# Performance work log

Hardware: AMD Instinct MI355X
Metric: run time of the kernel (lower is better)

Reference implementation:

```python
import jax, jax.numpy as jnp
import numpy as np

N = 65536      # total nodes
E = 262144     # directed edges
G = 2048       # graphs in batch
H = 512        # hidden_channels
HEADS = 2
DESC = 256


def setup_inputs() -> dict:
    key = jax.random.key(0)
    ks = jax.random.split(key, 18)
    w = lambda k, shape: (jax.random.normal(k, shape, jnp.float32) * 0.05)
    x = jax.random.normal(ks[0], (N, 9), jnp.float32)
    edge_index = jax.random.randint(ks[1], (2, E), 0, N)
    batch_index = (jnp.arange(N) * G) // N  # sorted graph ids, every graph non-empty
    descriptors = jax.random.normal(ks[2], (G, DESC), jnp.float32)
    return dict(
        x=x, edge_index=edge_index, batch_index=batch_index, descriptors=descriptors,
        gin_w=w(ks[3], (H, 9)), gin_b=w(ks[4], (H,)),
        gat_w=w(ks[5], (HEADS * H, H)), gat_asrc=w(ks[6], (HEADS, H)),
        gat_adst=w(ks[7], (HEADS, H)), gat_bias=w(ks[8], (H,)),
        sage_wl=w(ks[9], (H, H)), sage_bl=w(ks[10], (H,)), sage_wr=w(ks[11], (H, H)),
        fc_w=w(ks[12], (512, 2 * H + DESC)), fc_b=w(ks[13], (512,)),
        a1_w=w(ks[14], (256, 512)), a1_b=w(ks[15], (256,)),
        a2_w=w(ks[16], (1, 256)), a2_b=w(ks[17], (1,)),
    )


def reference(x, edge_index, batch_index, descriptors,
              gin_w, gin_b, gat_w, gat_asrc, gat_adst, gat_bias,
              sage_wl, sage_bl, sage_wr, fc_w, fc_b, a1_w, a1_b, a2_w, a2_b):
    # Dropout layers are identity in eval mode.
    gelu = lambda t: jax.nn.gelu(t, approximate=False)
    src, dst = edge_index[0], edge_index[1]

    # --- GINConv: nn((1+eps)*x + sum_{j->i} x_j), eps=0 ---
    agg = jax.ops.segment_sum(x[src], dst, num_segments=N)
    h = gelu((x + agg) @ gin_w.T + gin_b)

    # --- GATConv (heads=2, concat=False, add_self_loops=True) ---
    z = (h @ gat_w.T).reshape(N, HEADS, H)               # [N, heads, H]
    sl = jnp.arange(N)
    s2 = jnp.concatenate([src, sl])                      # edges + self loops
    d2 = jnp.concatenate([dst, sl])
    a_s = jnp.sum(z * gat_asrc[None], axis=-1)           # [N, heads]
    a_d = jnp.sum(z * gat_adst[None], axis=-1)
    logit = jax.nn.leaky_relu(a_s[s2] + a_d[d2], 0.2)    # [E', heads]
    m = jax.ops.segment_max(logit, d2, num_segments=N)
    e = jnp.exp(logit - m[d2])
    denom = jax.ops.segment_sum(e, d2, num_segments=N)
    alpha = e / denom[d2]                                # edge softmax per dst
    out = jax.ops.segment_sum(alpha[:, :, None] * z[s2], d2, num_segments=N)
    h = gelu(out.mean(axis=1) + gat_bias)

    # --- SAGEConv: lin_l(mean_j h_j) + lin_r(h_i) ---
    cnt = jax.ops.segment_sum(jnp.ones((E,), h.dtype), dst, num_segments=N)
    mean_agg = jax.ops.segment_sum(h[src], dst, num_segments=N) / jnp.maximum(cnt, 1.0)[:, None]
    h = gelu(mean_agg @ sage_wl.T + sage_bl + h @ sage_wr.T)

    # --- global max/mean pool + heads ---
    pmax = jax.ops.segment_max(h, batch_index, num_segments=G)
    nodes_per_g = jax.ops.segment_sum(jnp.ones((N,), h.dtype), batch_index, num_segments=G)
    pmean = jax.ops.segment_sum(h, batch_index, num_segments=G) / nodes_per_g[:, None]
    combined = jnp.concatenate([pmax, pmean, descriptors], axis=1)  # [G, 2H+DESC]
    sf = gelu(combined @ fc_w.T + fc_b)
    z1 = gelu(sf @ a1_w.T + a1_b)
    return z1 @ a2_w.T + a2_b                             # [G, 1]
```

## Files before the change

kernel.cpp:

```cpp
#include <hip/hip_runtime.h>
#include <math.h>

#define N_NODES 65536
#define N_EDGES 262144
#define N_GRAPHS 2048
#define HDIM 512
#define DESCD 256

typedef unsigned short u16;
typedef __attribute__((ext_vector_type(8))) short bf16x8;
typedef __attribute__((ext_vector_type(8))) u16 u16x8;
typedef __attribute__((ext_vector_type(4))) float f32x4;

__device__ __forceinline__ float gelu_f(float x) {
    return 0.5f * x * (1.0f + erff(x * 0.70710678118654752f));
}
__device__ __forceinline__ float lrelu_f(float x) {
    return x > 0.0f ? x : 0.2f * x;
}
__device__ __forceinline__ float wave_reduce_sum(float v) {
#pragma unroll
    for (int off = 32; off > 0; off >>= 1) v += __shfl_down(v, off, 64);
    return v;
}

__device__ __forceinline__ float bf2f(u16 u) { return __uint_as_float(((unsigned)u) << 16); }
__device__ __forceinline__ u16 f2bf(float f) {
    unsigned u = __float_as_uint(f);
    unsigned r = (u >> 16) & 1u;
    return (u16)((u + 0x7fffu + r) >> 16);
}
__device__ __forceinline__ void ld8b(const u16* p, float o[8]) {
    ushort4 v0 = *(const ushort4*)p;
    ushort4 v1 = *(const ushort4*)(p + 4);
    o[0] = bf2f(v0.x); o[1] = bf2f(v0.y); o[2] = bf2f(v0.z); o[3] = bf2f(v0.w);
    o[4] = bf2f(v1.x); o[5] = bf2f(v1.y); o[6] = bf2f(v1.z); o[7] = bf2f(v1.w);
}
__device__ __forceinline__ void st8b(u16* p, const float o[8]) {
    ushort4 a, b;
    a.x = f2bf(o[0]); a.y = f2bf(o[1]); a.z = f2bf(o[2]); a.w = f2bf(o[3]);
    b.x = f2bf(o[4]); b.y = f2bf(o[5]); b.z = f2bf(o[6]); b.w = f2bf(o[7]);
    *(ushort4*)p = a; *(ushort4*)(p + 4) = b;
}

__global__ void k_zero(int* __restrict__ p, int n) {
    int i = blockIdx.x * blockDim.x + threadIdx.x;
    if (i < n) p[i] = 0;
}

__global__ void k_cvt(const float* __restrict__ src, u16* __restrict__ dst, int n) {
    int i = blockIdx.x * blockDim.x + threadIdx.x;
    if (i < n) dst[i] = f2bf(src[i]);
}

__global__ void k_count(const int* __restrict__ dst, int* __restrict__ deg) {
    int e = blockIdx.x * blockDim.x + threadIdx.x;
    if (e < N_EDGES) atomicAdd(&deg[dst[e]], 1);
}

__global__ __launch_bounds__(1024) void k_scan(const int* __restrict__ deg,
                                               int* __restrict__ indptr,
                                               int* __restrict__ cursor) {
    __shared__ int part[1024];
    int t = threadIdx.x;
    int base = t * 64;
    int s = 0;
    for (int i = 0; i < 64; i++) s += deg[base + i];
    part[t] = s;
    __syncthreads();
    for (int off = 1; off < 1024; off <<= 1) {
        int v = (t >= off) ? part[t - off] : 0;
        __syncthreads();
        part[t] += v;
        __syncthreads();
    }
    int run = (t == 0) ? 0 : part[t - 1];
    for (int i = 0; i < 64; i++) {
        int d = deg[base + i];
        indptr[base + i] = run;
        cursor[base + i] = run;
        run += d;
    }
    if (t == 1023) indptr[N_NODES] = run;
}

__global__ void k_fill(const int* __restrict__ src, const int* __restrict__ dst,
                       int* __restrict__ cursor, int* __restrict__ col) {
    int e = blockIdx.x * blockDim.x + threadIdx.x;
    if (e < N_EDGES) {
        int d = dst[e];
        int pos = atomicAdd(&cursor[d], 1);
        col[pos] = src[e];
    }
}

__global__ __launch_bounds__(256) void k_gin(const float* __restrict__ x,
                                             const int* __restrict__ indptr,
                                             const int* __restrict__ col,
                                             const float* __restrict__ gw,
                                             const float* __restrict__ gb,
                                             u16* __restrict__ h1) {
    __shared__ float w[HDIM * 9];
    __shared__ float b[HDIM];
    for (int idx = threadIdx.x; idx < HDIM * 9; idx += 256) w[idx] = gw[idx];
    for (int idx = threadIdx.x; idx < HDIM; idx += 256) b[idx] = gb[idx];
    __syncthreads();
    int wave = threadIdx.x >> 6, lane = threadIdx.x & 63;
    int i = blockIdx.x * 4 + wave;
    if (i >= N_NODES) return;
    float s[9];
#pragma unroll
    for (int k = 0; k < 9; k++) s[k] = x[i * 9 + k];
    int beg = indptr[i], end = indptr[i + 1];
    for (int e = beg; e < end; e++) {
        int j = col[e];
#pragma unroll
        for (int k = 0; k < 9; k++) s[k] += x[j * 9 + k];
    }
#pragma unroll
    for (int q = 0; q < 8; q++) {
        int c = q * 64 + lane;
        float acc = b[c];
#pragma unroll
        for (int k = 0; k < 9; k++) acc += s[k] * w[c * 9 + k];
        h1[(size_t)i * HDIM + c] = f2bf(gelu_f(acc));
    }
}

__global__ __launch_bounds__(256) void k_vproj(const float* __restrict__ gat_w,
                                               const float* __restrict__ asrc,
                                               const float* __restrict__ adst,
                                               float* __restrict__ vs,
                                               float* __restrict__ vd) {
    int h = blockIdx.x;
    int t = threadIdx.x;
    const float* W = gat_w + (size_t)h * HDIM * HDIM;
    float s0 = 0.f, s1 = 0.f, d0 = 0.f, d1 = 0.f;
    for (int c = 0; c < HDIM; c++) {
        float as = asrc[h * HDIM + c], ad = adst[h * HDIM + c];
        float w0 = W[(size_t)c * HDIM + t];
        float w1 = W[(size_t)c * HDIM + t + 256];
        s0 += as * w0; s1 += as * w1;
        d0 += ad * w0; d1 += ad * w1;
    }
    vs[h * HDIM + t] = s0; vs[h * HDIM + t + 256] = s1;
    vd[h * HDIM + t] = d0; vd[h * HDIM + t + 256] = d1;
}

__global__ __launch_bounds__(256) void k_coef(const u16* __restrict__ h1,
                                              const float* __restrict__ vs,
                                              const float* __restrict__ vd,
                                              float* __restrict__ a_s,
                                              float* __restrict__ a_d) {
    int wave = threadIdx.x >> 6, lane = threadIdx.x & 63;
    int i = blockIdx.x * 4 + wave;
    if (i >= N_NODES) return;
    float hv[8];
    ld8b(h1 + (size_t)i * HDIM + lane * 8, hv);
    float s0 = 0, d0 = 0, s1 = 0, d1 = 0;
#pragma unroll
    for (int r = 0; r < 8; r++) {
        int c = lane * 8 + r;
        s0 += hv[r] * vs[c];
        d0 += hv[r] * vd[c];
        s1 += hv[r] * vs[HDIM + c];
        d1 += hv[r] * vd[HDIM + c];
    }
    s0 = wave_reduce_sum(s0);
    d0 = wave_reduce_sum(d0);
    s1 = wave_reduce_sum(s1);
    d1 = wave_reduce_sum(d1);
    if (lane == 0) {
        a_s[i * 2] = s0; a_s[i * 2 + 1] = s1;
        a_d[i * 2] = d0; a_d[i * 2 + 1] = d1;
    }
}

__global__ __launch_bounds__(256) void k_gatagg(const u16* __restrict__ h1,
                                                const float* __restrict__ a_s,
                                                const float* __restrict__ a_d,
                                                const int* __restrict__ indptr,
                                                const int* __restrict__ col,
                                                u16* __restrict__ agg0,
                                                u16* __restrict__ agg1) {
    int wave = threadIdx.x >> 6, lane = threadIdx.x & 63;
    int i = blockIdx.x * 4 + wave;
    if (i >= N_NODES) return;
    int beg = indptr[i], end = indptr[i + 1];
    float ad0 = a_d[i * 2], ad1 = a_d[i * 2 + 1];
    float sl0 = expf(lrelu_f(a_s[i * 2] + ad0));
    float sl1 = expf(lrelu_f(a_s[i * 2 + 1] + ad1));
    float den0 = sl0, den1 = sl1;
    for (int e = beg; e < end; e++) {
        int j = col[e];
        den0 += expf(lrelu_f(a_s[j * 2] + ad0));
        den1 += expf(lrelu_f(a_s[j * 2 + 1] + ad1));
    }
    float inv0 = 0.5f / den0, inv1 = 0.5f / den1;
    float acc0[8], acc1[8], hv[8];
    ld8b(h1 + (size_t)i * HDIM + lane * 8, hv);
    {
        float w0 = sl0 * inv0, w1 = sl1 * inv1;
#pragma unroll
        for (int r = 0; r < 8; r++) { acc0[r] = w0 * hv[r]; acc1[r] = w1 * hv[r]; }
    }
    for (int e = beg; e < end; e++) {
        int j = col[e];
        float w0 = expf(lrelu_f(a_s[j * 2] + ad0)) * inv0;
        float w1 = expf(lrelu_f(a_s[j * 2 + 1] + ad1)) * inv1;
        ld8b(h1 + (size_t)j * HDIM + lane * 8, hv);
#pragma unroll
        for (int r = 0; r < 8; r++) { acc0[r] += w0 * hv[r]; acc1[r] += w1 * hv[r]; }
    }
    st8b(agg0 + (size_t)i * HDIM + lane * 8, acc0);
    st8b(agg1 + (size_t)i * HDIM + lane * 8, acc1);
}

template <bool DUAL, bool POOL, bool AF32>
__global__ __launch_bounds__(256) void k_mgemm(const void* __restrict__ A0v,
                                               const u16* __restrict__ W0,
                                               const void* __restrict__ A1v,
                                               const u16* __restrict__ W1,
                                               int K, const float* __restrict__ bias,
                                               u16* __restrict__ C, int ldc,
                                               float* __restrict__ comb) {
    __shared__ u16 sA[128 * 64];
    __shared__ u16 sB[128 * 64];
    int t = threadIdx.x;
    int wave = t >> 6, lane = t & 63;
    int wr = wave >> 1, wc = wave & 1;
    int l15 = lane & 15, l4 = lane >> 4;
    int bx, by;
    {
        int nwgx = gridDim.x;
        int nwg = nwgx * gridDim.y;
        int bid = blockIdx.y * nwgx + blockIdx.x;
        int q = nwg >> 3;
        int l = (bid & 7) * q + (bid >> 3);
        bx = l % nwgx;
        by = l / nwgx;
    }
    int row0 = by * 128;
    int c0 = bx * 128;

    f32x4 acc[4][4];
#pragma unroll
    for (int i = 0; i < 4; i++)
#pragma unroll
        for (int j = 0; j < 4; j++) acc[i][j] = (f32x4){0.f, 0.f, 0.f, 0.f};

    int half = K / 64;
    int nks = DUAL ? 2 * half : half;
    for (int ks = 0; ks < nks; ks++) {
        bool second = DUAL && (ks >= half);
        const u16* ApU = (const u16*)(second ? A1v : A0v);
        const float* ApF = (const float*)(second ? A1v : A0v);
        const u16* Wp = second ? W1 : W0;
        int k0 = (second ? (ks - half) : ks) * 64;
        u16x8 ga[4], gb[4];
#pragma unroll
        for (int q = 0; q < 4; q++) {
            int cid = q * 256 + t;
            int row = cid >> 3, cb = cid & 7;
            if constexpr (AF32) {
                const float* p = ApF + (size_t)(row0 + row) * K + k0 + cb * 8;
                float4 f0 = *(const float4*)p;
                float4 f1 = *(const float4*)(p + 4);
                u16x8 v;
                v[0] = f2bf(f0.x); v[1] = f2bf(f0.y); v[2] = f2bf(f0.z); v[3] = f2bf(f0.w);
                v[4] = f2bf(f1.x); v[5] = f2bf(f1.y); v[6] = f2bf(f1.z); v[7] = f2bf(f1.w);
                ga[q] = v;
            } else {
                ga[q] = *(const u16x8*)(ApU + (size_t)(row0 + row) * K + k0 + cb * 8);
            }
            gb[q] = *(const u16x8*)(Wp + (size_t)(c0 + row) * K + k0 + cb * 8);
        }
        __syncthreads();
#pragma unroll
        for (int q = 0; q < 4; q++) {
            int cid = q * 256 + t;
            int row = cid >> 3, cb = cid & 7;
            int sw = (cb ^ (row & 7)) * 8;
            *(u16x8*)(sA + row * 64 + sw) = ga[q];
            *(u16x8*)(sB + row * 64 + sw) = gb[q];
        }
        __syncthreads();
#pragma unroll
        for (int h = 0; h < 2; h++) {
            bf16x8 af[4], bfv[4];
            int cb = h * 4 + l4;
#pragma unroll
            for (int i = 0; i < 4; i++) {
                int ra = wr * 64 + i * 16 + l15;
                af[i] = *(const bf16x8*)(sA + ra * 64 + ((cb ^ (ra & 7)) * 8));
                int rb = wc * 64 + i * 16 + l15;
                bfv[i] = *(const bf16x8*)(sB + rb * 64 + ((cb ^ (rb & 7)) * 8));
            }
#pragma unroll
            for (int i = 0; i < 4; i++)
#pragma unroll
                for (int j = 0; j < 4; j++)
                    acc[i][j] = __builtin_amdgcn_mfma_f32_16x16x32_bf16(af[i], bfv[j], acc[i][j], 0, 0, 0);
        }
    }

    if constexpr (!POOL) {
#pragma unroll
        for (int i = 0; i < 4; i++) {
            int rbase = row0 + wr * 64 + i * 16 + l4 * 4;
#pragma unroll
            for (int j = 0; j < 4; j++) {
                int colc = c0 + wc * 64 + j * 16 + l15;
                float bv = bias[colc];
#pragma unroll
                for (int r = 0; r < 4; r++)
                    C[(size_t)(rbase + r) * ldc + colc] = f2bf(gelu_f(acc[i][j][r] + bv));
            }
        }
    } else {
#pragma unroll
        for (int gl = 0; gl < 2; gl++) {
            int g = (row0 >> 5) + wr * 2 + gl;
#pragma unroll
            for (int j = 0; j < 4; j++) {
                int colc = c0 + wc * 64 + j * 16 + l15;
                float bv = bias[colc];
                float mx = -1e30f, sm = 0.0f;
#pragma unroll
                for (int i = 0; i < 2; i++) {
#pragma unroll
                    for (int r = 0; r < 4; r++) {
                        float v = gelu_f(acc[gl * 2 + i][j][r] + bv);
                        mx = fmaxf(mx, v);
                        sm += v;
                    }
                }
                mx = fmaxf(mx, __shfl_xor(mx, 16, 64)); sm += __shfl_xor(sm, 16, 64);
                mx = fmaxf(mx, __shfl_xor(mx, 32, 64)); sm += __shfl_xor(sm, 32, 64);
                if (l4 == 0) {
                    comb[(size_t)g * 1280 + colc] = mx;
                    comb[(size_t)g * 1280 + 512 + colc] = sm * (1.0f / 32.0f);
                }
            }
        }
    }
}

__global__ __launch_bounds__(256) void k_sagemean(const u16* __restrict__ h2,
                                                  const int* __restrict__ indptr,
                                                  const int* __restrict__ col,
                                                  u16* __restrict__ mean) {
    int wave = threadIdx.x >> 6, lane = threadIdx.x & 63;
    int i = blockIdx.x * 4 + wave;
    if (i >= N_NODES) return;
    int beg = indptr[i], end = indptr[i + 1];
    float acc[8], hv[8];
#pragma unroll
    for (int r = 0; r < 8; r++) acc[r] = 0.0f;
    for (int e = beg; e < end; e++) {
        int j = col[e];
        ld8b(h2 + (size_t)j * HDIM + lane * 8, hv);
#pragma unroll
        for (int r = 0; r < 8; r++) acc[r] += hv[r];
    }
    float invc = 1.0f / fmaxf((float)(end - beg), 1.0f);
#pragma unroll
    for (int r = 0; r < 8; r++) acc[r] *= invc;
    st8b(mean + (size_t)i * HDIM + lane * 8, acc);
}

__global__ void k_desc(const float* __restrict__ desc, float* __restrict__ comb) {
    int idx = blockIdx.x * blockDim.x + threadIdx.x;
    int g = idx >> 8, c = idx & 255;
    comb[(size_t)g * 1280 + 1024 + c] = desc[(size_t)g * DESCD + c];
}

__global__ __launch_bounds__(256) void k_final(const u16* __restrict__ z1,
                                               const float* __restrict__ a2w,
                                               const float* __restrict__ a2b,
                                               float* __restrict__ out) {
    int wave = threadIdx.x >> 6, lane = threadIdx.x & 63;
    int g = blockIdx.x * 4 + wave;
    if (g >= N_GRAPHS) return;
    float s = 0.0f;
#pragma unroll
    for (int q = 0; q < 4; q++) {
        int c = q * 64 + lane;
        s += bf2f(z1[g * 256 + c]) * a2w[c];
    }
    s = wave_reduce_sum(s);
    if (lane == 0) out[g] = s + a2b[0];
}

extern "C" void kernel_launch(void* const* d_in, const int* in_sizes, int n_in,
                              void* d_out, int out_size, void* d_ws, size_t ws_size,
                              hipStream_t stream) {
    (void)in_sizes; (void)n_in;
    const float* x = (const float*)d_in[0];
    const int* ei = (const int*)d_in[1];
    const int* src = ei;
    const int* dst = ei + N_EDGES;
    const float* desc = (const float*)d_in[3];
    const float* gin_w = (const float*)d_in[4];
    const float* gin_b = (const float*)d_in[5];
    const float* gat_w = (const float*)d_in[6];
    const float* gat_asrc = (const float*)d_in[7];
    const float* gat_adst = (const float*)d_in[8];
    const float* gat_bias = (const float*)d_in[9];
    const float* sage_wl = (const float*)d_in[10];
    const float* sage_bl = (const float*)d_in[11];
    const float* sage_wr = (const float*)d_in[12];
    const float* fc_w = (const float*)d_in[13];
    const float* fc_b = (const float*)d_in[14];
    const float* a1_w = (const float*)d_in[15];
    const float* a1_b = (const float*)d_in[16];
    const float* a2_w = (const float*)d_in[17];
    const float* a2_b = (const float*)d_in[18];
    float* out = (float*)d_out;

    if (ws_size < (size_t)200 * 1024 * 1024) {
        k_zero<<<(out_size + 255) / 256, 256, 0, stream>>>((int*)d_out, out_size);
        return;
    }

    char* wsp = (char*)d_ws;
    auto alloc = [&](size_t bytes) {
        char* p = wsp;
        wsp += (bytes + 255) & ~(size_t)255;
        return p;
    };
    int* deg = (int*)alloc((size_t)N_NODES * 4);
    int* indptr = (int*)alloc((size_t)(N_NODES + 1) * 4);
    int* cursor = (int*)alloc((size_t)N_NODES * 4);
    int* colv = (int*)alloc((size_t)N_EDGES * 4);
    float* a_s = (float*)alloc((size_t)N_NODES * 2 * 4);
    float* a_d = (float*)alloc((size_t)N_NODES * 2 * 4);
    float* vs = (float*)alloc((size_t)2 * HDIM * 4);
    float* vd = (float*)alloc((size_t)2 * HDIM * 4);
    u16* Wb = (u16*)alloc(((size_t)4 * HDIM * HDIM + 512 * 1280 + 256 * 512) * 2);
    size_t nodeb = (size_t)N_NODES * HDIM * 2;
    u16* R1 = (u16*)alloc(nodeb);
    u16* R2 = (u16*)alloc(nodeb);
    u16* R3 = (u16*)alloc(nodeb);

    float* comb = (float*)R3;
    u16* sf = (u16*)(comb + (size_t)N_GRAPHS * 1280);
    u16* z1 = sf + (size_t)N_GRAPHS * 512;

    u16* Wb0 = Wb;
    u16* Wb1 = Wb + (size_t)HDIM * HDIM;
    u16* Wb2 = Wb1 + (size_t)HDIM * HDIM;
    u16* Wb3 = Wb2 + (size_t)HDIM * HDIM;
    u16* Wbfc = Wb3 + (size_t)HDIM * HDIM;
    u16* Wba1 = Wbfc + (size_t)512 * 1280;

    k_cvt<<<(2 * 262144 + 255) / 256, 256, 0, stream>>>(gat_w, Wb0, 2 * 262144);
    k_cvt<<<(262144 + 255) / 256, 256, 0, stream>>>(sage_wl, Wb2, 262144);
    k_cvt<<<(262144 + 255) / 256, 256, 0, stream>>>(sage_wr, Wb3, 262144);
    k_cvt<<<(655360 + 255) / 256, 256, 0, stream>>>(fc_w, Wbfc, 655360);
    k_cvt<<<(131072 + 255) / 256, 256, 0, stream>>>(a1_w, Wba1, 131072);

    k_zero<<<N_NODES / 256, 256, 0, stream>>>(deg, N_NODES);
    k_count<<<N_EDGES / 256, 256, 0, stream>>>(dst, deg);
    k_scan<<<1, 1024, 0, stream>>>(deg, indptr, cursor);
    k_fill<<<N_EDGES / 256, 256, 0, stream>>>(src, dst, cursor, colv);

    k_gin<<<N_NODES / 4, 256, 0, stream>>>(x, indptr, colv, gin_w, gin_b, R1);

    k_vproj<<<2, 256, 0, stream>>>(gat_w, gat_asrc, gat_adst, vs, vd);
    k_coef<<<N_NODES / 4, 256, 0, stream>>>(R1, vs, vd, a_s, a_d);

    k_gatagg<<<N_NODES / 4, 256, 0, stream>>>(R1, a_s, a_d, indptr, colv, R2, R3);

    k_mgemm<true, false, false><<<dim3(HDIM / 128, N_NODES / 128), 256, 0, stream>>>(
        R2, Wb0, R3, Wb1, HDIM, gat_bias, R1, HDIM, nullptr);

    k_sagemean<<<N_NODES / 4, 256, 0, stream>>>(R1, indptr, colv, R2);

    k_mgemm<true, true, false><<<dim3(HDIM / 128, N_NODES / 128), 256, 0, stream>>>(
        R2, Wb2, R1, Wb3, HDIM, sage_bl, nullptr, 0, comb);
    k_desc<<<N_GRAPHS, 256, 0, stream>>>(desc, comb);

    k_mgemm<false, false, true><<<dim3(512 / 128, N_GRAPHS / 128), 256, 0, stream>>>(
        comb, Wbfc, nullptr, nullptr, 1280, fc_b, sf, 512, nullptr);

    k_mgemm<false, false, false><<<dim3(256 / 128, N_GRAPHS / 128), 256, 0, stream>>>(
        sf, Wba1, nullptr, nullptr, HDIM, a1_b, z1, 256, nullptr);

    k_final<<<N_GRAPHS / 4, 256, 0, stream>>>(z1, a2_w, a2_b, out);
}
```

Measured before the change: 687.2 us.

## Fuse GAT coefficient pass into GIN, batch weight conversion, use direct global-to-LDS loads

Merges the five weight-conversion launches into one kernel. Folds the GAT attention-coefficient dot products into the GIN kernel so h1 is not re-read. Replaces register-staged global loads in the MFMA GEMM with global_load_lds for bf16 operands, with the XOR swizzle applied on the global side. These cut launch overhead, one full pass over node features, and register staging in the GEMM. The cost is extra work and register pressure inside the GIN kernel, plus the risk that the LDS load addressing does not match the swizzled read layout.

```diff
diff --git a/kernel.cpp b/kernel.cpp
--- a/kernel.cpp
+++ b/kernel.cpp
@@ -12,6 +12,11 @@
 typedef __attribute__((ext_vector_type(8))) u16 u16x8;
 typedef __attribute__((ext_vector_type(4))) float f32x4;
 
+#define GLD_LDS(g, l)                                                          \
+    __builtin_amdgcn_global_load_lds(                                          \
+        (const __attribute__((address_space(1))) unsigned int*)(g),            \
+        (__attribute__((address_space(3))) unsigned int*)(l), 16, 0, 0)
+
 __device__ __forceinline__ float gelu_f(float x) {
     return 0.5f * x * (1.0f + erff(x * 0.70710678118654752f));
 }
@@ -48,9 +53,21 @@
     if (i < n) p[i] = 0;
 }
 
-__global__ void k_cvt(const float* __restrict__ src, u16* __restrict__ dst, int n) {
-    int i = blockIdx.x * blockDim.x + threadIdx.x;
-    if (i < n) dst[i] = f2bf(src[i]);
+__global__ void k_cvtall(const float* __restrict__ gat_w,
+                         const float* __restrict__ sage_wl,
+                         const float* __restrict__ sage_wr,
+                         const float* __restrict__ fc_w,
+                         const float* __restrict__ a1_w,
+                         u16* __restrict__ Wb) {
+    int id = blockIdx.x * 256 + threadIdx.x;
+    const float* src;
+    int off;
+    if (id < 524288) { src = gat_w; off = id; }
+    else if (id < 786432) { src = sage_wl; off = id - 524288; }
+    else if (id < 1048576) { src = sage_wr; off = id - 786432; }
+    else if (id < 1703936) { src = fc_w; off = id - 1048576; }
+    else { src = a1_w; off = id - 1703936; }
+    Wb[id] = f2bf(src[off]);
 }
 
 __global__ void k_count(const int* __restrict__ dst, int* __restrict__ deg) {
@@ -94,39 +111,6 @@
     }
 }
 
-__global__ __launch_bounds__(256) void k_gin(const float* __restrict__ x,
-                                             const int* __restrict__ indptr,
-                                             const int* __restrict__ col,
-                                             const float* __restrict__ gw,
-                                             const float* __restrict__ gb,
-                                             u16* __restrict__ h1) {
-    __shared__ float w[HDIM * 9];
-    __shared__ float b[HDIM];
-    for (int idx = threadIdx.x; idx < HDIM * 9; idx += 256) w[idx] = gw[idx];
-    for (int idx = threadIdx.x; idx < HDIM; idx += 256) b[idx] = gb[idx];
-    __syncthreads();
-    int wave = threadIdx.x >> 6, lane = threadIdx.x & 63;
-    int i = blockIdx.x * 4 + wave;
-    if (i >= N_NODES) return;
-    float s[9];
-#pragma unroll
-    for (int k = 0; k < 9; k++) s[k] = x[i * 9 + k];
-    int beg = indptr[i], end = indptr[i + 1];
-    for (int e = beg; e < end; e++) {
-        int j = col[e];
-#pragma unroll
-        for (int k = 0; k < 9; k++) s[k] += x[j * 9 + k];
-    }
-#pragma unroll
-    for (int q = 0; q < 8; q++) {
-        int c = q * 64 + lane;
-        float acc = b[c];
-#pragma unroll
-        for (int k = 0; k < 9; k++) acc += s[k] * w[c * 9 + k];
-        h1[(size_t)i * HDIM + c] = f2bf(gelu_f(acc));
-    }
-}
-
 __global__ __launch_bounds__(256) void k_vproj(const float* __restrict__ gat_w,
                                                const float* __restrict__ asrc,
                                                const float* __restrict__ adst,
@@ -147,24 +131,46 @@
     vd[h * HDIM + t] = d0; vd[h * HDIM + t + 256] = d1;
 }
 
-__global__ __launch_bounds__(256) void k_coef(const u16* __restrict__ h1,
-                                              const float* __restrict__ vs,
-                                              const float* __restrict__ vd,
-                                              float* __restrict__ a_s,
-                                              float* __restrict__ a_d) {
+__global__ __launch_bounds__(256) void k_gin(const float* __restrict__ x,
+                                             const int* __restrict__ indptr,
+                                             const int* __restrict__ col,
+                                             const float* __restrict__ gw,
+                                             const float* __restrict__ gb,
+                                             const float* __restrict__ vs,
+                                             const float* __restrict__ vd,
+                                             u16* __restrict__ h1,
+                                             float* __restrict__ a_s,
+                                             float* __restrict__ a_d) {
+    __shared__ float w[HDIM * 9];
+    __shared__ float b[HDIM];
+    for (int idx = threadIdx.x; idx < HDIM * 9; idx += 256) w[idx] = gw[idx];
+    for (int idx = threadIdx.x; idx < HDIM; idx += 256) b[idx] = gb[idx];
+    __syncthreads();
     int wave = threadIdx.x >> 6, lane = threadIdx.x & 63;
     int i = blockIdx.x * 4 + wave;
     if (i >= N_NODES) return;
-    float hv[8];
-    ld8b(h1 + (size_t)i * HDIM + lane * 8, hv);
+    float s[9];
+#pragma unroll
+    for (int k = 0; k < 9; k++) s[k] = x[i * 9 + k];
+    int beg = indptr[i], end = indptr[i + 1];
+    for (int e = beg; e < end; e++) {
+        int j = col[e];
+#pragma unroll
+        for (int k = 0; k < 9; k++) s[k] += x[j * 9 + k];
+    }
     float s0 = 0, d0 = 0, s1 = 0, d1 = 0;
 #pragma unroll
-    for (int r = 0; r < 8; r++) {
-        int c = lane * 8 + r;
-        s0 += hv[r] * vs[c];
-        d0 += hv[r] * vd[c];
-        s1 += hv[r] * vs[HDIM + c];
-        d1 += hv[r] * vd[HDIM + c];
+    for (int q = 0; q < 8; q++) {
+        int c = q * 64 + lane;
+        float acc = b[c];
+#pragma unroll
+        for (int k = 0; k < 9; k++) acc += s[k] * w[c * 9 + k];
+        float v = gelu_f(acc);
+        h1[(size_t)i * HDIM + c] = f2bf(v);
+        s0 += v * vs[c];
+        d0 += v * vd[c];
+        s1 += v * vs[HDIM + c];
+        d1 += v * vd[HDIM + c];
     }
     s0 = wave_reduce_sum(s0);
     d0 = wave_reduce_sum(d0);
@@ -243,6 +249,9 @@
     int row0 = by * 128;
     int c0 = bx * 128;
 
+    int rowoff = lane >> 3;
+    int gchunk = (lane & 7) ^ rowoff;
+
     f32x4 acc[4][4];
 #pragma unroll
     for (int i = 0; i < 4; i++)
@@ -257,12 +266,13 @@
         const float* ApF = (const float*)(second ? A1v : A0v);
         const u16* Wp = second ? W1 : W0;
         int k0 = (second ? (ks - half) : ks) * 64;
-        u16x8 ga[4], gb[4];
-#pragma unroll
-        for (int q = 0; q < 4; q++) {
-            int cid = q * 256 + t;
-            int row = cid >> 3, cb = cid & 7;
-            if constexpr (AF32) {
+
+        u16x8 ga[4];
+        if constexpr (AF32) {
+#pragma unroll
+            for (int q = 0; q < 4; q++) {
+                int cid = q * 256 + t;
+                int row = cid >> 3, cb = cid & 7;
                 const float* p = ApF + (size_t)(row0 + row) * K + k0 + cb * 8;
                 float4 f0 = *(const float4*)p;
                 float4 f1 = *(const float4*)(p + 4);
@@ -270,19 +280,29 @@
                 v[0] = f2bf(f0.x); v[1] = f2bf(f0.y); v[2] = f2bf(f0.z); v[3] = f2bf(f0.w);
                 v[4] = f2bf(f1.x); v[5] = f2bf(f1.y); v[6] = f2bf(f1.z); v[7] = f2bf(f1.w);
                 ga[q] = v;
-            } else {
-                ga[q] = *(const u16x8*)(ApU + (size_t)(row0 + row) * K + k0 + cb * 8);
             }
-            gb[q] = *(const u16x8*)(Wp + (size_t)(c0 + row) * K + k0 + cb * 8);
         }
         __syncthreads();
+        if constexpr (AF32) {
+#pragma unroll
+            for (int q = 0; q < 4; q++) {
+                int cid = q * 256 + t;
+                int row = cid >> 3, cb = cid & 7;
+                *(u16x8*)(sA + row * 64 + ((cb ^ (row & 7)) * 8)) = ga[q];
+            }
+        } else {
+#pragma unroll
+            for (int q = 0; q < 4; q++) {
+                int r0 = wave * 32 + q * 8;
+                GLD_LDS(ApU + (size_t)(row0 + r0 + rowoff) * K + k0 + gchunk * 8,
+                        sA + r0 * 64);
+            }
+        }
 #pragma unroll
         for (int q = 0; q < 4; q++) {
-            int cid = q * 256 + t;
-            int row = cid >> 3, cb = cid & 7;
-            int sw = (cb ^ (row & 7)) * 8;
-            *(u16x8*)(sA + row * 64 + sw) = ga[q];
-            *(u16x8*)(sB + row * 64 + sw) = gb[q];
+            int r0 = wave * 32 + q * 8;
+            GLD_LDS(Wp + (size_t)(c0 + r0 + rowoff) * K + k0 + gchunk * 8,
+                    sB + r0 * 64);
         }
         __syncthreads();
 #pragma unroll
@@ -437,7 +457,7 @@
     float* a_d = (float*)alloc((size_t)N_NODES * 2 * 4);
     float* vs = (float*)alloc((size_t)2 * HDIM * 4);
     float* vd = (float*)alloc((size_t)2 * HDIM * 4);
-    u16* Wb = (u16*)alloc(((size_t)4 * HDIM * HDIM + 512 * 1280 + 256 * 512) * 2);
+    u16* Wb = (u16*)alloc((size_t)1835008 * 2);
     size_t nodeb = (size_t)N_NODES * HDIM * 2;
     u16* R1 = (u16*)alloc(nodeb);
     u16* R2 = (u16*)alloc(nodeb);
@@ -448,27 +468,23 @@
     u16* z1 = sf + (size_t)N_GRAPHS * 512;
 
     u16* Wb0 = Wb;
-    u16* Wb1 = Wb + (size_t)HDIM * HDIM;
-    u16* Wb2 = Wb1 + (size_t)HDIM * HDIM;
-    u16* Wb3 = Wb2 + (size_t)HDIM * HDIM;
-    u16* Wbfc = Wb3 + (size_t)HDIM * HDIM;
-    u16* Wba1 = Wbfc + (size_t)512 * 1280;
-
-    k_cvt<<<(2 * 262144 + 255) / 256, 256, 0, stream>>>(gat_w, Wb0, 2 * 262144);
-    k_cvt<<<(262144 + 255) / 256, 256, 0, stream>>>(sage_wl, Wb2, 262144);
-    k_cvt<<<(262144 + 255) / 256, 256, 0, stream>>>(sage_wr, Wb3, 262144);
-    k_cvt<<<(655360 + 255) / 256, 256, 0, stream>>>(fc_w, Wbfc, 655360);
-    k_cvt<<<(131072 + 255) / 256, 256, 0, stream>>>(a1_w, Wba1, 131072);
+    u16* Wb1 = Wb + 262144;
+    u16* Wb2 = Wb + 524288;
+    u16* Wb3 = Wb + 786432;
+    u16* Wbfc = Wb + 1048576;
+    u16* Wba1 = Wb + 1703936;
+
+    k_cvtall<<<7168, 256, 0, stream>>>(gat_w, sage_wl, sage_wr, fc_w, a1_w, Wb);
 
     k_zero<<<N_NODES / 256, 256, 0, stream>>>(deg, N_NODES);
     k_count<<<N_EDGES / 256, 256, 0, stream>>>(dst, deg);
     k_scan<<<1, 1024, 0, stream>>>(deg, indptr, cursor);
     k_fill<<<N_EDGES / 256, 256, 0, stream>>>(src, dst, cursor, colv);
 
-    k_gin<<<N_NODES / 4, 256, 0, stream>>>(x, indptr, colv, gin_w, gin_b, R1);
-
     k_vproj<<<2, 256, 0, stream>>>(gat_w, gat_asrc, gat_adst, vs, vd);
-    k_coef<<<N_NODES / 4, 256, 0, stream>>>(R1, vs, vd, a_s, a_d);
+
+    k_gin<<<N_NODES / 4, 256, 0, stream>>>(x, indptr, colv, gin_w, gin_b, vs, vd,
+                                           R1, a_s, a_d);
 
     k_gatagg<<<N_NODES / 4, 256, 0, stream>>>(R1, a_s, a_d, indptr, colv, R2, R3);
 
```

Measured after the change: 679.5 us. No clear change (-1.1%).
